# Kernel tuning notes

Measured on AMD Instinct MI355X. Metric: run time of the kernel, lower is better.

Reference implementation:

```python
import jax, jax.numpy as jnp
import numpy as np

N_NODES = 100000
N_EDGES = 1200000
NFEAT, NHID, NCLASS = 64, 256, 40
DROP_RATE = 0.5
ORDER = 8


def setup_inputs() -> dict:
    key = jax.random.key(0)
    k = jax.random.split(key, 6)
    x = jax.random.normal(k[0], (N_NODES, NFEAT), dtype=jnp.float32)
    edge_index = jax.random.randint(k[1], (2, N_EDGES), 0, N_NODES, dtype=jnp.int64)
    stdv1 = 1.0 / np.sqrt(NHID)
    stdv2 = 1.0 / np.sqrt(NCLASS)
    W1 = jax.random.normal(k[2], (NFEAT, NHID), dtype=jnp.float32) * stdv1
    b1 = jax.random.normal(k[3], (NHID,), dtype=jnp.float32) * stdv1
    W2 = jax.random.normal(k[4], (NHID, NCLASS), dtype=jnp.float32) * stdv2
    b2 = jax.random.normal(k[5], (NCLASS,), dtype=jnp.float32) * stdv2
    return {"x": x, "edge_index": edge_index, "W1": W1, "b1": b1, "W2": W2, "b2": b2}


def _norm_adj(edge_index, n):
    # A + I, then D^{-1/2} (A+I) D^{-1/2}  (GCN symmetric normalization)
    loops = jnp.arange(n, dtype=edge_index.dtype)
    row = jnp.concatenate([edge_index[0], loops])
    col = jnp.concatenate([edge_index[1], loops])
    ones = jnp.ones(row.shape[0], dtype=jnp.float32)
    deg = jax.ops.segment_sum(ones, row, num_segments=n)  # row sums (self-loops guarantee deg>=1)
    d_inv_sqrt = 1.0 / jnp.sqrt(deg)
    ew = d_inv_sqrt[row] * d_inv_sqrt[col]  # [E+N] edge weights
    return row, col, ew


def reference(x, edge_index, W1, b1, W2, b2):
    n = x.shape[0]
    row, col, ew = _norm_adj(edge_index, n)

    def spmm(h):  # out[row] += ew * h[col]
        return jax.ops.segment_sum(ew[:, None] * h[col], row, num_segments=n)

    # eval-mode input scaling (training=False branch of GRAND.forward)
    h = x * (1.0 - DROP_RATE)
    y = h
    for _ in range(ORDER):
        h = spmm(h)
        y = y + h
    y = y / (ORDER + 1.0)

    # MLP in eval mode: dropouts are no-ops, use_bn=False
    hid = jax.nn.relu(y @ W1 + b1)
    return hid @ W2 + b2
```

## Files before the change

kernel.cpp:

```cpp
#include <hip/hip_runtime.h>

#define NN 100000
#define NE 1200000
#define NF 64
#define NH 256
#define NC 40
#define ORDER_C 8
#define SC 1024
#define BINB 1024
#define BCAP 165000
#define CCAP (NE + 7 * NN)

typedef __attribute__((ext_vector_type(8))) short short8;
typedef __attribute__((ext_vector_type(4))) float f32x4;

__device__ __forceinline__ unsigned bf16r(float x) {
    unsigned u = __float_as_uint(x);
    return (u + 0x7FFFu + ((u >> 16) & 1u)) >> 16;
}
__device__ __forceinline__ unsigned packbf(float lo, float hi) {
    return bf16r(lo) | (bf16r(hi) << 16);
}
__device__ __forceinline__ float bflo(unsigned u) { return __uint_as_float(u << 16); }
__device__ __forceinline__ float bfhi(unsigned u) { return __uint_as_float(u & 0xFFFF0000u); }


static __global__ __launch_bounds__(256) void k_bin(const int* __restrict__ rows,
                                                    const int* __restrict__ cols,
                                                    int* __restrict__ bcnt,
                                                    int* __restrict__ browb,
                                                    int* __restrict__ bcolb, int E)
{
    __shared__ int rbuf[BINB];
    __shared__ unsigned short lofs[BINB];
    __shared__ int hist[8], basew[8];
    int t = threadIdx.x;
    int e0 = blockIdx.x * BINB;
    int m = E - e0; if (m > BINB) m = BINB;
    if (t < 8) hist[t] = 0;
    __syncthreads();
    for (int i = t; i < m; i += 256) {
        int r = rows[e0 + i];
        rbuf[i] = r;
        int b = r / 12500;
        lofs[i] = (unsigned short)atomicAdd(&hist[b], 1);
    }
    __syncthreads();
    if (t < 8) basew[t] = atomicAdd(&bcnt[t], hist[t]);
    __syncthreads();
    for (int i = t; i < m; i += 256) {
        int r = rbuf[i];
        int b = r / 12500;
        size_t pos = (size_t)b * BCAP + basew[b] + lofs[i];
        browb[pos] = r;
        bcolb[pos] = cols[e0 + i];
    }
}


static __global__ __launch_bounds__(256) void k_cnt2(const int* __restrict__ browb,
                                                     const int* __restrict__ bcnt,
                                                     int* __restrict__ cnt)
{
    int grp = blockIdx.x & 7;
    int m = bcnt[grp];
    const int* src = browb + (size_t)grp * BCAP;
    int stride = (gridDim.x >> 3) * 256;
    for (int i = (blockIdx.x >> 3) * 256 + threadIdx.x; i < m; i += stride)
        atomicAdd(&cnt[src[i]], 1);
}


static __global__ __launch_bounds__(256) void k_bsum(const int* __restrict__ cnt,
                                                     int* __restrict__ bsum, int n)
{
    __shared__ int red[256];
    int t = threadIdx.x;
    int idx = blockIdx.x * SC + t * 4;
    int s = 0;
    if (idx + 3 < n) {
        int4 q = *(const int4*)&cnt[idx];
        s = ((q.x + 7) & ~7) + ((q.y + 7) & ~7) + ((q.z + 7) & ~7) + ((q.w + 7) & ~7);
    } else {
        for (int j = 0; j < 4; ++j) if (idx + j < n) s += (cnt[idx + j] + 7) & ~7;
    }
    red[t] = s;
    __syncthreads();
    for (int off = 128; off > 0; off >>= 1) {
        if (t < off) red[t] += red[t + off];
        __syncthreads();
    }
    if (t == 0) bsum[blockIdx.x] = red[0];
}

static __global__ __launch_bounds__(128) void k_scanb(const int* __restrict__ bsum,
                                                      int* __restrict__ boff,
                                                      int* __restrict__ rp, int nb, int n)
{
    __shared__ int red[128];
    int t = threadIdx.x;
    int v = (t < nb) ? bsum[t] : 0;
    red[t] = v;
    __syncthreads();
    for (int off = 1; off < 128; off <<= 1) {
        int x = (t >= off) ? red[t - off] : 0;
        __syncthreads();
        red[t] += x;
        __syncthreads();
    }
    if (t < nb) boff[t] = (t == 0) ? 0 : red[t - 1];
    if (t == 0) rp[n] = red[127];
}

static __global__ __launch_bounds__(256) void k_scan3(const int* __restrict__ cnt,
                                                      const int* __restrict__ boff,
                                                      int* __restrict__ rp,
                                                      float2* __restrict__ drd, int n)
{
    __shared__ int red[256];
    int t = threadIdx.x;
    int idx = blockIdx.x * SC + t * 4;
    int v[4] = {0, 0, 0, 0};
    if (idx + 3 < n) {
        int4 q = *(const int4*)&cnt[idx];
        v[0] = q.x; v[1] = q.y; v[2] = q.z; v[3] = q.w;
    } else {
        for (int j = 0; j < 4; ++j) if (idx + j < n) v[j] = cnt[idx + j];
    }
    int p[4];
    #pragma unroll
    for (int j = 0; j < 4; ++j) p[j] = (v[j] + 7) & ~7;
    red[t] = p[0] + p[1] + p[2] + p[3];
    __syncthreads();
    for (int off = 1; off < 256; off <<= 1) {
        int x = (t >= off) ? red[t - off] : 0;
        __syncthreads();
        red[t] += x;
        __syncthreads();
    }
    int run = ((t == 0) ? 0 : red[t - 1]) + boff[blockIdx.x];
    #pragma unroll
    for (int j = 0; j < 4; ++j) {
        if (idx + j < n) {
            rp[idx + j] = run;
            float d1 = rsqrtf((float)(v[j] + 1));
            drd[idx + j] = make_float2(d1, (float)(v[j] + 1) * d1);
            run += p[j];
        }
    }
}


static __global__ __launch_bounds__(256) void k_fillc(int4* __restrict__ ccol4, int cap4, int val)
{
    int i = blockIdx.x * 256 + threadIdx.x;
    if (i < cap4) ccol4[i] = make_int4(val, val, val, val);
}


static __global__ __launch_bounds__(256) void k_scat2(const int* __restrict__ browb,
                                                      const int* __restrict__ bcolb,
                                                      const int* __restrict__ bcnt,
                                                      int* __restrict__ fillpos,
                                                      int* __restrict__ ccol)
{
    int grp = blockIdx.x & 7;
    int m = bcnt[grp];
    const int* srcr = browb + (size_t)grp * BCAP;
    const int* srcc = bcolb + (size_t)grp * BCAP;
    int stride = (gridDim.x >> 3) * 256;
    for (int i = (blockIdx.x >> 3) * 256 + threadIdx.x; i < m; i += stride) {
        int r = srcr[i];
        int pos = atomicAdd(&fillpos[r], 1);
        ccol[pos] = srcc[i];
    }
}


static __global__ __launch_bounds__(256) void k_pack(const float* __restrict__ W1,
                                                     const float* __restrict__ W2,
                                                     unsigned short* __restrict__ w1f,
                                                     unsigned short* __restrict__ w2f)
{
    int t = blockIdx.x * 256 + threadIdx.x;
    if (t < 2048) {
        int lane = t & 63;
        int g = lane >> 4, col = (lane & 15) + ((t >> 6) & 15) * 16;
        int s = t >> 10;
        unsigned short* p = w1f + (size_t)t * 8;
        #pragma unroll
        for (int e = 0; e < 8; ++e) {
            int k = 32 * s + 8 * g + e;
            p[e] = (unsigned short)bf16r(W1[k * NH + col]);
        }
    } else if (t < 2048 + 1536) {
        int u = t - 2048;
        int lane = u & 63;
        int tile = u >> 6;
        int nt = tile % 3, s = tile / 3;
        int g = lane >> 4, col = (lane & 15) + nt * 16;
        unsigned short* p = w2f + (size_t)u * 8;
        #pragma unroll
        for (int e = 0; e < 8; ++e) {
            int k = 32 * s + 8 * g + e;
            p[e] = (col < NC) ? (unsigned short)bf16r(W2[k * NC + col]) : 0;
        }
    }
}


static __global__ __launch_bounds__(256) void k_init(const float4* __restrict__ x4,
                                                     float4* __restrict__ y4,
                                                     uint4* __restrict__ ga,
                                                     uint4* __restrict__ gbp,
                                                     const float2* __restrict__ drd,
                                                     int nchunk)
{
    int i = blockIdx.x * 256 + threadIdx.x;
    if (i >= nchunk) {
        if (i < nchunk + 8) {
            uint4 z = make_uint4(0, 0, 0, 0);
            ga[i] = z; gbp[i] = z;
        }
        return;
    }
    float d1 = drd[i >> 3].x;
    float4 a = x4[i * 2], b = x4[i * 2 + 1];
    a.x *= 0.5f; a.y *= 0.5f; a.z *= 0.5f; a.w *= 0.5f;
    b.x *= 0.5f; b.y *= 0.5f; b.z *= 0.5f; b.w *= 0.5f;
    y4[i * 2] = a; y4[i * 2 + 1] = b;
    ga[i] = make_uint4(packbf(a.x * d1, a.y * d1), packbf(a.z * d1, a.w * d1),
                       packbf(b.x * d1, b.y * d1), packbf(b.z * d1, b.w * d1));
}


template<bool ACC>
static __global__ __launch_bounds__(256) void k_spmm(const uint2* __restrict__ gb,
                                                     uint2* __restrict__ go,
                                                     float4* __restrict__ y4,
                                                     const int* __restrict__ rp,
                                                     const int* __restrict__ ccol,
                                                     const float2* __restrict__ drd, int n)
{
    int wid  = (blockIdx.x * 256 + threadIdx.x) >> 6;
    int lane = threadIdx.x & 63;
    int row  = wid * 4 + (lane >> 4);
    int j    = lane & 15;
    if (row >= n) return;
    int s = rp[row], e = rp[row + 1];

    float a0 = 0.f, a1 = 0.f, a2 = 0.f, a3 = 0.f;
    float b0 = 0.f, b1 = 0.f, b2 = 0.f, b3 = 0.f;
    for (int i = s; i < e; i += 8) {
        int4 cA = *(const int4*)&ccol[i];
        int4 cB = *(const int4*)&ccol[i + 4];
        uint2 h0 = gb[(size_t)cA.x * 16 + j];
        uint2 h1 = gb[(size_t)cA.y * 16 + j];
        uint2 h2 = gb[(size_t)cA.z * 16 + j];
        uint2 h3 = gb[(size_t)cA.w * 16 + j];
        uint2 h4 = gb[(size_t)cB.x * 16 + j];
        uint2 h5 = gb[(size_t)cB.y * 16 + j];
        uint2 h6 = gb[(size_t)cB.z * 16 + j];
        uint2 h7 = gb[(size_t)cB.w * 16 + j];
        a0 += bflo(h0.x); a1 += bfhi(h0.x); a2 += bflo(h0.y); a3 += bfhi(h0.y);
        b0 += bflo(h1.x); b1 += bfhi(h1.x); b2 += bflo(h1.y); b3 += bfhi(h1.y);
        a0 += bflo(h2.x); a1 += bfhi(h2.x); a2 += bflo(h2.y); a3 += bfhi(h2.y);
        b0 += bflo(h3.x); b1 += bfhi(h3.x); b2 += bflo(h3.y); b3 += bfhi(h3.y);
        a0 += bflo(h4.x); a1 += bfhi(h4.x); a2 += bflo(h4.y); a3 += bfhi(h4.y);
        b0 += bflo(h5.x); b1 += bfhi(h5.x); b2 += bflo(h5.y); b3 += bfhi(h5.y);
        a0 += bflo(h6.x); a1 += bfhi(h6.x); a2 += bflo(h6.y); a3 += bfhi(h6.y);
        b0 += bflo(h7.x); b1 += bfhi(h7.x); b2 += bflo(h7.y); b3 += bfhi(h7.y);
    }

    float2 dr = drd[row];
    uint2 gs = gb[(size_t)row * 16 + j];
    float g0 = bflo(gs.x), g1 = bfhi(gs.x), g2 = bflo(gs.y), g3 = bfhi(gs.y);
    float s0 = (a0 + b0) + g0;
    float s1 = (a1 + b1) + g1;
    float s2 = (a2 + b2) + g2;
    float s3 = (a3 + b3) + g3;
    float h0 = dr.x * s0, h1 = dr.x * s1, h2 = dr.x * s2, h3 = dr.x * s3;
    go[(size_t)row * 16 + j] = make_uint2(packbf(dr.x * h0, dr.x * h1),
                                          packbf(dr.x * h2, dr.x * h3));
    if (ACC) {
        float4 yv = y4[(size_t)row * 16 + j];
        yv.x += fmaf(g0, dr.y, h0);
        yv.y += fmaf(g1, dr.y, h1);
        yv.z += fmaf(g2, dr.y, h2);
        yv.w += fmaf(g3, dr.y, h3);
        y4[(size_t)row * 16 + j] = yv;
    }
}


#define YSTR 72
#define HSTR 264

static __global__ __launch_bounds__(256) void k_mlp(const float4* __restrict__ y4,
                                                    const short8* __restrict__ w1f,
                                                    const short8* __restrict__ w2f,
                                                    const float* __restrict__ b1,
                                                    const float* __restrict__ b2,
                                                    float* __restrict__ out, int n)
{
    __shared__ short lds[64 * HSTR];
    int t = threadIdx.x;
    int lane = t & 63;
    int w = t >> 6;
    int base = blockIdx.x * 64;
    const float S = 1.f / 9.f;

    {
        int r = t >> 2, q = t & 3;
        int row = base + r;
        unsigned v[8];
        if (row < n) {
            const float4* yp = y4 + (size_t)row * 16 + q * 4;
            #pragma unroll
            for (int i = 0; i < 4; ++i) {
                float4 f = yp[i];
                v[i * 2]     = packbf(f.x * S, f.y * S);
                v[i * 2 + 1] = packbf(f.z * S, f.w * S);
            }
        } else {
            #pragma unroll
            for (int i = 0; i < 8; ++i) v[i] = 0;
        }
        uint4* dst = (uint4*)&lds[r * YSTR + q * 16];
        dst[0] = make_uint4(v[0], v[1], v[2], v[3]);
        dst[1] = make_uint4(v[4], v[5], v[6], v[7]);
    }
    __syncthreads();

    int m = lane & 15, g = lane >> 4;

    f32x4 acc[4][4];
    {
        short8 a[4][2];
        #pragma unroll
        for (int mt = 0; mt < 4; ++mt)
            #pragma unroll
            for (int s = 0; s < 2; ++s)
                a[mt][s] = *(const short8*)&lds[(mt * 16 + m) * YSTR + s * 32 + g * 8];
        #pragma unroll
        for (int nt4 = 0; nt4 < 4; ++nt4) {
            int nt = w * 4 + nt4;
            short8 b0  = w1f[nt * 64 + lane];
            short8 b1v = w1f[(16 + nt) * 64 + lane];
            float bias = b1[nt * 16 + m];
            #pragma unroll
            for (int mt = 0; mt < 4; ++mt) {
                f32x4 c = {bias, bias, bias, bias};
                c = __builtin_amdgcn_mfma_f32_16x16x32_bf16(a[mt][0], b0,  c, 0, 0, 0);
                c = __builtin_amdgcn_mfma_f32_16x16x32_bf16(a[mt][1], b1v, c, 0, 0, 0);
                acc[mt][nt4] = c;
            }
        }
    }
    __syncthreads();

    {
        #pragma unroll
        for (int mt = 0; mt < 4; ++mt)
            #pragma unroll
            for (int nt4 = 0; nt4 < 4; ++nt4) {
                int col = w * 64 + nt4 * 16 + m;
                #pragma unroll
                for (int r = 0; r < 4; ++r) {
                    float hv = fmaxf(acc[mt][nt4][r], 0.f);
                    lds[(mt * 16 + g * 4 + r) * HSTR + col] = (short)bf16r(hv);
                }
            }
    }
    __syncthreads();

    {
        short8 a2[8];
        #pragma unroll
        for (int s = 0; s < 8; ++s)
            a2[s] = *(const short8*)&lds[(w * 16 + m) * HSTR + s * 32 + g * 8];
        #pragma unroll
        for (int nt = 0; nt < 3; ++nt) {
            int col = nt * 16 + m;
            float bias = (col < NC) ? b2[col] : 0.f;
            f32x4 c = {bias, bias, bias, bias};
            #pragma unroll
            for (int s = 0; s < 8; ++s)
                c = __builtin_amdgcn_mfma_f32_16x16x32_bf16(a2[s], w2f[(s * 3 + nt) * 64 + lane], c, 0, 0, 0);
            if (col < NC) {
                #pragma unroll
                for (int r = 0; r < 4; ++r) {
                    int row = base + w * 16 + g * 4 + r;
                    if (row < n) out[(size_t)row * NC + col] = c[r];
                }
            }
        }
    }
}


extern "C" void kernel_launch(void* const* d_in, const int* in_sizes, int n_in,
                              void* d_out, int out_size, void* d_ws, size_t ws_size,
                              hipStream_t stream)
{
    const float* x  = (const float*)d_in[0];
    const int*   ei = (const int*)d_in[1];
    const float* W1 = (const float*)d_in[2];
    const float* b1 = (const float*)d_in[3];
    const float* W2 = (const float*)d_in[4];
    const float* b2 = (const float*)d_in[5];
    float* out = (float*)d_out;

    const int n = NN, E = NE;
    const int nb = (n + SC - 1) / SC;

    char* ws = (char*)d_ws;
    size_t off = 0;
    auto alloc = [&](size_t bytes) -> void* {
        void* p = ws + off;
        off = (off + bytes + 255) & ~(size_t)255;
        return p;
    };
    int*    cnt   = (int*)   alloc((size_t)n * 4);
    int*    fill  = (int*)   alloc((size_t)n * 4);
    int*    rp    = (int*)   alloc((size_t)(n + 1) * 4);
    float2* drd   = (float2*)alloc((size_t)n * 8);
    int*    bsum  = (int*)   alloc(128 * 4);
    int*    boff  = (int*)   alloc(128 * 4);
    int*    bcnt  = (int*)   alloc(8 * 4);
    int*    browb = (int*)   alloc((size_t)8 * BCAP * 4);
    int*    bcolb = (int*)   alloc((size_t)8 * BCAP * 4);
    int*    ccol  = (int*)   alloc((size_t)CCAP * 4);
    unsigned short* w1f = (unsigned short*)alloc(2048 * 8 * 2);
    unsigned short* w2f = (unsigned short*)alloc(1536 * 8 * 2);
    uint4* ha   = (uint4*)alloc((size_t)(n + 1) * NF * 2);
    uint4* hbuf = (uint4*)alloc((size_t)(n + 1) * NF * 2);
    float* y    = (float*)alloc((size_t)n * NF * 4);

    hipMemsetAsync(cnt, 0, (size_t)n * 4, stream);
    hipMemsetAsync(bcnt, 0, 8 * 4, stream);

    const int* rows = ei;
    const int* cols = ei + E;

    k_bin   <<<(E + BINB - 1) / BINB, 256, 0, stream>>>(rows, cols, bcnt, browb, bcolb, E);
    k_cnt2  <<<4096, 256, 0, stream>>>(browb, bcnt, cnt);
    k_bsum  <<<nb, 256, 0, stream>>>(cnt, bsum, n);
    k_scanb <<<1, 128, 0, stream>>>(bsum, boff, rp, nb, n);
    k_scan3 <<<nb, 256, 0, stream>>>(cnt, boff, rp, drd, n);
    hipMemcpyAsync(fill, rp, (size_t)n * 4, hipMemcpyDeviceToDevice, stream);
    k_fillc <<<(CCAP / 4 + 255) / 256, 256, 0, stream>>>((int4*)ccol, CCAP / 4, n);
    k_scat2 <<<4096, 256, 0, stream>>>(browb, bcolb, bcnt, fill, ccol);
    k_pack  <<<14, 256, 0, stream>>>(W1, W2, w1f, w2f);

    int nchunk = n * 8;
    k_init<<<(nchunk + 8 + 255) / 256, 256, 0, stream>>>((const float4*)x, (float4*)y,
                                                         ha, hbuf, drd, nchunk);

    uint4* cur = ha;
    uint4* nxt = hbuf;
    int spmm_blocks = (n + 15) / 16;
    for (int it = 0; it < ORDER_C; ++it) {
        if (it & 1)
            k_spmm<true><<<spmm_blocks, 256, 0, stream>>>((const uint2*)cur, (uint2*)nxt,
                                                          (float4*)y, rp, ccol, drd, n);
        else
            k_spmm<false><<<spmm_blocks, 256, 0, stream>>>((const uint2*)cur, (uint2*)nxt,
                                                           (float4*)y, rp, ccol, drd, n);
        uint4* tswap = cur; cur = nxt; nxt = tswap;
    }

    k_mlp<<<(n + 63) / 64, 256, 0, stream>>>((const float4*)y, (const short8*)w1f,
                                             (const short8*)w2f, b1, b2, out, n);
}
```

Baseline: 405.9 us.

## Vectorize atomics loops, fuse ccol padding into scan, skip last g write, unroll spmm

The count and scatter kernels now read four row indices per thread with int4 loads and use smaller grids. The separate kernel that fills the whole ccol buffer is removed, and each row's padding slots are written inside the scan kernel instead. The final SpMM iteration no longer writes the unused g output. A 16-wide unrolled gather path is added for iterations where (it>>1)&1 holds. These are several loosely related changes to cut launches, redundant writes and loop overhead, at the cost of more register pressure in the unrolled variant.

```diff
diff --git a/kernel.cpp b/kernel.cpp
--- a/kernel.cpp
+++ b/kernel.cpp
@@ -65,9 +65,17 @@
     int grp = blockIdx.x & 7;
     int m = bcnt[grp];
     const int* src = browb + (size_t)grp * BCAP;
+    int nquad = m >> 2;
     int stride = (gridDim.x >> 3) * 256;
-    for (int i = (blockIdx.x >> 3) * 256 + threadIdx.x; i < m; i += stride)
-        atomicAdd(&cnt[src[i]], 1);
+    for (int q = (blockIdx.x >> 3) * 256 + threadIdx.x; q < nquad; q += stride) {
+        int4 r4 = *(const int4*)&src[q * 4];
+        atomicAdd(&cnt[r4.x], 1);
+        atomicAdd(&cnt[r4.y], 1);
+        atomicAdd(&cnt[r4.z], 1);
+        atomicAdd(&cnt[r4.w], 1);
+    }
+    if ((blockIdx.x >> 3) == 0 && threadIdx.x < (m & 3))
+        atomicAdd(&cnt[src[nquad * 4 + threadIdx.x]], 1);
 }
 
 
@@ -115,7 +123,8 @@
 static __global__ __launch_bounds__(256) void k_scan3(const int* __restrict__ cnt,
                                                       const int* __restrict__ boff,
                                                       int* __restrict__ rp,
-                                                      float2* __restrict__ drd, int n)
+                                                      float2* __restrict__ drd,
+                                                      int* __restrict__ ccol, int n)
 {
     __shared__ int red[256];
     int t = threadIdx.x;
@@ -145,16 +154,10 @@
             rp[idx + j] = run;
             float d1 = rsqrtf((float)(v[j] + 1));
             drd[idx + j] = make_float2(d1, (float)(v[j] + 1) * d1);
+            for (int q = v[j]; q < p[j]; ++q) ccol[run + q] = n;
             run += p[j];
         }
     }
-}
-
-
-static __global__ __launch_bounds__(256) void k_fillc(int4* __restrict__ ccol4, int cap4, int val)
-{
-    int i = blockIdx.x * 256 + threadIdx.x;
-    if (i < cap4) ccol4[i] = make_int4(val, val, val, val);
 }
 
 
@@ -168,10 +171,23 @@
     int m = bcnt[grp];
     const int* srcr = browb + (size_t)grp * BCAP;
     const int* srcc = bcolb + (size_t)grp * BCAP;
+    int nquad = m >> 2;
     int stride = (gridDim.x >> 3) * 256;
-    for (int i = (blockIdx.x >> 3) * 256 + threadIdx.x; i < m; i += stride) {
-        int r = srcr[i];
-        int pos = atomicAdd(&fillpos[r], 1);
+    for (int q = (blockIdx.x >> 3) * 256 + threadIdx.x; q < nquad; q += stride) {
+        int4 r4 = *(const int4*)&srcr[q * 4];
+        int4 c4 = *(const int4*)&srcc[q * 4];
+        int p0 = atomicAdd(&fillpos[r4.x], 1);
+        int p1 = atomicAdd(&fillpos[r4.y], 1);
+        int p2 = atomicAdd(&fillpos[r4.z], 1);
+        int p3 = atomicAdd(&fillpos[r4.w], 1);
+        ccol[p0] = c4.x;
+        ccol[p1] = c4.y;
+        ccol[p2] = c4.z;
+        ccol[p3] = c4.w;
+    }
+    if ((blockIdx.x >> 3) == 0 && threadIdx.x < (m & 3)) {
+        int i = nquad * 4 + threadIdx.x;
+        int pos = atomicAdd(&fillpos[srcr[i]], 1);
         ccol[pos] = srcc[i];
     }
 }
@@ -234,7 +250,7 @@
 }
 
 
-template<bool ACC>
+template<bool ACC, bool WRITEG, bool U16>
 static __global__ __launch_bounds__(256) void k_spmm(const uint2* __restrict__ gb,
                                                      uint2* __restrict__ go,
                                                      float4* __restrict__ y4,
@@ -251,7 +267,48 @@
 
     float a0 = 0.f, a1 = 0.f, a2 = 0.f, a3 = 0.f;
     float b0 = 0.f, b1 = 0.f, b2 = 0.f, b3 = 0.f;
-    for (int i = s; i < e; i += 8) {
+    int i = s;
+    if (U16) {
+        for (; i + 15 < e; i += 16) {
+            int4 cA = *(const int4*)&ccol[i];
+            int4 cB = *(const int4*)&ccol[i + 4];
+            int4 cC = *(const int4*)&ccol[i + 8];
+            int4 cD = *(const int4*)&ccol[i + 12];
+            uint2 h0 = gb[(size_t)cA.x * 16 + j];
+            uint2 h1 = gb[(size_t)cA.y * 16 + j];
+            uint2 h2 = gb[(size_t)cA.z * 16 + j];
+            uint2 h3 = gb[(size_t)cA.w * 16 + j];
+            uint2 h4 = gb[(size_t)cB.x * 16 + j];
+            uint2 h5 = gb[(size_t)cB.y * 16 + j];
+            uint2 h6 = gb[(size_t)cB.z * 16 + j];
+            uint2 h7 = gb[(size_t)cB.w * 16 + j];
+            uint2 h8 = gb[(size_t)cC.x * 16 + j];
+            uint2 h9 = gb[(size_t)cC.y * 16 + j];
+            uint2 hA = gb[(size_t)cC.z * 16 + j];
+            uint2 hB = gb[(size_t)cC.w * 16 + j];
+            uint2 hC = gb[(size_t)cD.x * 16 + j];
+            uint2 hD = gb[(size_t)cD.y * 16 + j];
+            uint2 hE = gb[(size_t)cD.z * 16 + j];
+            uint2 hF = gb[(size_t)cD.w * 16 + j];
+            a0 += bflo(h0.x); a1 += bfhi(h0.x); a2 += bflo(h0.y); a3 += bfhi(h0.y);
+            b0 += bflo(h1.x); b1 += bfhi(h1.x); b2 += bflo(h1.y); b3 += bfhi(h1.y);
+            a0 += bflo(h2.x); a1 += bfhi(h2.x); a2 += bflo(h2.y); a3 += bfhi(h2.y);
+            b0 += bflo(h3.x); b1 += bfhi(h3.x); b2 += bflo(h3.y); b3 += bfhi(h3.y);
+            a0 += bflo(h4.x); a1 += bfhi(h4.x); a2 += bflo(h4.y); a3 += bfhi(h4.y);
+            b0 += bflo(h5.x); b1 += bfhi(h5.x); b2 += bflo(h5.y); b3 += bfhi(h5.y);
+            a0 += bflo(h6.x); a1 += bfhi(h6.x); a2 += bflo(h6.y); a3 += bfhi(h6.y);
+            b0 += bflo(h7.x); b1 += bfhi(h7.x); b2 += bflo(h7.y); b3 += bfhi(h7.y);
+            a0 += bflo(h8.x); a1 += bfhi(h8.x); a2 += bflo(h8.y); a3 += bfhi(h8.y);
+            b0 += bflo(h9.x); b1 += bfhi(h9.x); b2 += bflo(h9.y); b3 += bfhi(h9.y);
+            a0 += bflo(hA.x); a1 += bfhi(hA.x); a2 += bflo(hA.y); a3 += bfhi(hA.y);
+            b0 += bflo(hB.x); b1 += bfhi(hB.x); b2 += bflo(hB.y); b3 += bfhi(hB.y);
+            a0 += bflo(hC.x); a1 += bfhi(hC.x); a2 += bflo(hC.y); a3 += bfhi(hC.y);
+            b0 += bflo(hD.x); b1 += bfhi(hD.x); b2 += bflo(hD.y); b3 += bfhi(hD.y);
+            a0 += bflo(hE.x); a1 += bfhi(hE.x); a2 += bflo(hE.y); a3 += bfhi(hE.y);
+            b0 += bflo(hF.x); b1 += bfhi(hF.x); b2 += bflo(hF.y); b3 += bfhi(hF.y);
+        }
+    }
+    for (; i < e; i += 8) {
         int4 cA = *(const int4*)&ccol[i];
         int4 cB = *(const int4*)&ccol[i + 4];
         uint2 h0 = gb[(size_t)cA.x * 16 + j];
@@ -280,8 +337,9 @@
     float s2 = (a2 + b2) + g2;
     float s3 = (a3 + b3) + g3;
     float h0 = dr.x * s0, h1 = dr.x * s1, h2 = dr.x * s2, h3 = dr.x * s3;
-    go[(size_t)row * 16 + j] = make_uint2(packbf(dr.x * h0, dr.x * h1),
-                                          packbf(dr.x * h2, dr.x * h3));
+    if (WRITEG)
+        go[(size_t)row * 16 + j] = make_uint2(packbf(dr.x * h0, dr.x * h1),
+                                              packbf(dr.x * h2, dr.x * h3));
     if (ACC) {
         float4 yv = y4[(size_t)row * 16 + j];
         yv.x += fmaf(g0, dr.y, h0);
@@ -444,13 +502,12 @@
     const int* cols = ei + E;
 
     k_bin   <<<(E + BINB - 1) / BINB, 256, 0, stream>>>(rows, cols, bcnt, browb, bcolb, E);
-    k_cnt2  <<<4096, 256, 0, stream>>>(browb, bcnt, cnt);
+    k_cnt2  <<<2048, 256, 0, stream>>>(browb, bcnt, cnt);
     k_bsum  <<<nb, 256, 0, stream>>>(cnt, bsum, n);
     k_scanb <<<1, 128, 0, stream>>>(bsum, boff, rp, nb, n);
-    k_scan3 <<<nb, 256, 0, stream>>>(cnt, boff, rp, drd, n);
+    k_scan3 <<<nb, 256, 0, stream>>>(cnt, boff, rp, drd, ccol, n);
     hipMemcpyAsync(fill, rp, (size_t)n * 4, hipMemcpyDeviceToDevice, stream);
-    k_fillc <<<(CCAP / 4 + 255) / 256, 256, 0, stream>>>((int4*)ccol, CCAP / 4, n);
-    k_scat2 <<<4096, 256, 0, stream>>>(browb, bcolb, bcnt, fill, ccol);
+    k_scat2 <<<1024, 256, 0, stream>>>(browb, bcolb, bcnt, fill, ccol);
     k_pack  <<<14, 256, 0, stream>>>(W1, W2, w1f, w2f);
 
     int nchunk = n * 8;
@@ -461,12 +518,18 @@
     uint4* nxt = hbuf;
     int spmm_blocks = (n + 15) / 16;
     for (int it = 0; it < ORDER_C; ++it) {
-        if (it & 1)
-            k_spmm<true><<<spmm_blocks, 256, 0, stream>>>((const uint2*)cur, (uint2*)nxt,
-                                                          (float4*)y, rp, ccol, drd, n);
-        else
-            k_spmm<false><<<spmm_blocks, 256, 0, stream>>>((const uint2*)cur, (uint2*)nxt,
-                                                           (float4*)y, rp, ccol, drd, n);
+        bool acc = (it & 1) != 0;
+        bool u16 = ((it >> 1) & 1) != 0;
+        bool wg  = (it != ORDER_C - 1);
+        #define SPMM(A, W, U) k_spmm<A, W, U><<<spmm_blocks, 256, 0, stream>>>( \
+            (const uint2*)cur, (uint2*)nxt, (float4*)y, rp, ccol, drd, n)
+        if (acc) {
+            if (wg) { if (u16) SPMM(true, true, true); else SPMM(true, true, false); }
+            else    { if (u16) SPMM(true, false, true); else SPMM(true, false, false); }
+        } else {
+            if (u16) SPMM(false, true, true); else SPMM(false, true, false);
+        }
+        #undef SPMM
         uint4* tswap = cur; cur = nxt; nxt = tswap;
     }
 
```

Measured after the change: 406.0 us. No clear change (+0.0%).
